# Optimization experiments

Hardware: AMD Instinct MI355X
Metric: run time of the kernel (lower is better)

Reference implementation:

```python
import jax, jax.numpy as jnp
import numpy as np

MARGIN = 0.1
EPS = 1e-6  # torch CosineSimilarity eps


def setup_inputs() -> dict:
    key = jax.random.key(0)
    k1, k2 = jax.random.split(key)
    pred = jax.random.normal(k1, (8192, 512), dtype=jnp.float32)
    labels = jax.random.randint(k2, (8192,), 0, 14)  # one-hot gt <=> int labels
    return {"pred": pred, "labels": labels}


def _cosine(x, y):
    # torch.nn.CosineSimilarity(dim=1, eps=1e-6): clamp norms at eps
    nx = jnp.maximum(jnp.linalg.norm(x, axis=1), EPS)
    ny = jnp.maximum(jnp.linalg.norm(y, axis=1), EPS)
    return jnp.sum(x * y, axis=1) / (nx * ny)


def reference(pred, labels):
    B = pred.shape[0]
    # rows_pos: rows sharing the anchor's label (includes anchor itself, as in torch code)
    pos_mask = labels[:, None] == labels[None, :]  # [B, B] bool
    # random.sample(rows, 1) -> uniform random valid index per row, via gumbel-argmax
    kp, kn = jax.random.split(jax.random.key(42))
    neg_inf = jnp.float32(-1e30)
    g_pos = jax.random.gumbel(kp, (B, B), dtype=jnp.float32)
    g_neg = jax.random.gumbel(kn, (B, B), dtype=jnp.float32)
    idx_p = jnp.argmax(jnp.where(pos_mask, g_pos, neg_inf), axis=1)  # [B]
    idx_n = jnp.argmax(jnp.where(pos_mask, neg_inf, g_neg), axis=1)  # [B]

    anchor = pred
    positive = pred[idx_p]
    negative = pred[idx_n]
    cos_v = _cosine(anchor, positive) - _cosine(anchor, negative) + MARGIN
    return jnp.mean(jnp.maximum(cos_v, 0.0))
```

## Files before the change

### kernel.cpp

```cpp
#include <hip/hip_runtime.h>
#include <stdint.h>


#define B_ROWS 8192
#define DIMS   512
#define NLAB   16

__device__ __forceinline__ uint32_t rotl(uint32_t x, uint32_t r) {
  return __builtin_amdgcn_alignbit(x, x, 32u - r);
}

struct KeyPair { uint32_t a, b; };
constexpr KeyPair tf_c(uint32_t k0, uint32_t k1, uint32_t x0, uint32_t x1) {
  const uint32_t ks2 = k0 ^ k1 ^ 0x1BD11BDAu;
  x0 += k0; x1 += k1;
#define TFRC(r) { x0 += x1; x1 = (uint32_t)((x1 << (r)) | (x1 >> (32 - (r)))); x1 ^= x0; }
  TFRC(13) TFRC(15) TFRC(26) TFRC(6)
  x0 += k1;  x1 += ks2 + 1u;
  TFRC(17) TFRC(29) TFRC(16) TFRC(24)
  x0 += ks2; x1 += k0 + 2u;
  TFRC(13) TFRC(15) TFRC(26) TFRC(6)
  x0 += k0;  x1 += k1 + 3u;
  TFRC(17) TFRC(29) TFRC(16) TFRC(24)
  x0 += k1;  x1 += ks2 + 4u;
  TFRC(13) TFRC(15) TFRC(26) TFRC(6)
  x0 += ks2; x1 += k0 + 5u;
#undef TFRC
  return {x0, x1};
}
constexpr KeyPair KP = tf_c(0u, 42u, 0u, 0u);
constexpr KeyPair KN = tf_c(0u, 42u, 0u, 1u);

template <uint32_t K0, uint32_t K1>
__device__ __forceinline__ uint32_t tf_draw(uint32_t x1) {
  constexpr uint32_t KS2 = K0 ^ K1 ^ 0x1BD11BDAu;
  uint32_t x0 = K0 + x1;
  x1 = rotl(x1, 13); x1 ^= x0;
  x0 += x1; x1 = rotl(x1, 15); x1 ^= x0;
  x0 += x1; x1 = rotl(x1, 26); x1 ^= x0;
  x0 += x1; x1 = rotl(x1, 6);  x1 ^= x0;
  x1 += KS2 + 1u;  x0 = x0 + x1 + K1;
  x1 = rotl(x1, 17); x1 ^= x0;
  x0 += x1; x1 = rotl(x1, 29); x1 ^= x0;
  x0 += x1; x1 = rotl(x1, 16); x1 ^= x0;
  x0 += x1; x1 = rotl(x1, 24); x1 ^= x0;
  x1 += K0 + 2u;   x0 = x0 + x1 + KS2;
  x1 = rotl(x1, 13); x1 ^= x0;
  x0 += x1; x1 = rotl(x1, 15); x1 ^= x0;
  x0 += x1; x1 = rotl(x1, 26); x1 ^= x0;
  x0 += x1; x1 = rotl(x1, 6);  x1 ^= x0;
  x1 += K1 + 3u;   x0 = x0 + x1 + K0;
  x1 = rotl(x1, 17); x1 ^= x0;
  x0 += x1; x1 = rotl(x1, 29); x1 ^= x0;
  x0 += x1; x1 = rotl(x1, 16); x1 ^= x0;
  x0 += x1; x1 = rotl(x1, 24); x1 ^= x0;
  x1 += KS2 + 4u;  x0 = x0 + x1 + K1;
  x1 = rotl(x1, 13); x1 ^= x0;
  x0 += x1; x1 = rotl(x1, 15); x1 ^= x0;
  x0 += x1; x1 = rotl(x1, 26); x1 ^= x0;
  x0 += x1; x1 = rotl(x1, 6);  x1 ^= x0;
  return (x0 + KS2) ^ (x1 + K0 + 5u);
}

__global__ __launch_bounds__(256) void norms_sort_kernel(const float* __restrict__ pred,
                                                         const int* __restrict__ labels,
                                                         float* __restrict__ norms,
                                                         int* __restrict__ perm,
                                                         int* __restrict__ gstart) {
  __shared__ int cnt[NLAB][256];
  __shared__ int gs[NLAB + 1];
  const int wave = threadIdx.x >> 6, lane = threadIdx.x & 63;
  const int r = blockIdx.x * 4 + wave;
  const float4* A = (const float4*)(pred + (size_t)r * DIMS);
  float s = 0.f;
#pragma unroll
  for (int t = 0; t < 2; ++t) {
    const float4 a = A[lane + 64 * t];
    s += a.x * a.x + a.y * a.y + a.z * a.z + a.w * a.w;
  }
  for (int o = 32; o > 0; o >>= 1) s += __shfl_down(s, o, 64);
  if (lane == 0) norms[r] = sqrtf(s);

  if (blockIdx.x != 0) return;
  const int t = threadIdx.x;
  for (int l = 0; l < NLAB; ++l) cnt[l][t] = 0;
  __syncthreads();
  const int base = t * 32;
  for (int e = base; e < base + 32; ++e) cnt[labels[e]][t]++;
  __syncthreads();
  if (t < NLAB) {
    int run = 0;
    for (int k = 0; k < 256; ++k) { const int c = cnt[t][k]; cnt[t][k] = run; run += c; }
    gs[t + 1] = run;
  }
  __syncthreads();
  if (t == 0) {
    gs[0] = 0;
    for (int l = 1; l <= NLAB; ++l) gs[l] += gs[l - 1];
  }
  __syncthreads();
  for (int e = base; e < base + 32; ++e) {
    const int l = labels[e];
    perm[gs[l] + cnt[l][t]++] = e;
  }
  if (t <= NLAB) gstart[t] = gs[t];
}

__global__ __launch_bounds__(256) void argmax_kernel(const int* __restrict__ labels,
                                                     const int* __restrict__ perm,
                                                     const int* __restrict__ gstart,
                                                     int* __restrict__ idxp,
                                                     int* __restrict__ idxn) {
  __shared__ uint32_t labw[B_ROWS / 4];
  const int tid = threadIdx.x;
  {
    const int4* L4 = (const int4*)labels;
#pragma unroll
    for (int q = 0; q < 8; ++q) {
      const int4 a = L4[tid * 8 + q];
      labw[tid * 8 + q] = (uint32_t)a.x | ((uint32_t)a.y << 8) |
                          ((uint32_t)a.z << 16) | ((uint32_t)a.w << 24);
    }
  }
  const int lane = tid & 63;
  const int r = blockIdx.x * 4 + (tid >> 6);
  const int li = __builtin_amdgcn_readfirstlane(labels[r]);
  const int g0 = __builtin_amdgcn_readfirstlane(gstart[li]);
  const int g1 = __builtin_amdgcn_readfirstlane(gstart[li + 1]);
  const uint32_t base = (uint32_t)r << 13;

  int bv = -1, bj = 0;
  {
    const uint32_t sb = base + KP.b;
    for (int t = g0 + lane; t < g1; t += 64) {
      const int j = perm[t];
      const uint32_t w = tf_draw<KP.a, KP.b>(sb + (uint32_t)j);
      const int v = (int)(w >> 9);
      const bool upd = v > bv;
      bv = upd ? v : bv;
      bj = upd ? j : bj;
    }
  }
  unsigned long long pp =
      (((unsigned long long)(bv + 1)) << 13) | (unsigned)(8191 - bj);

  __syncthreads();

  bv = -1; bj = 0;
  {
    const uint8_t* lb = (const uint8_t*)labw;
    uint32_t x1w = base + KN.b + (uint32_t)lane;
    int jw = lane;
#pragma unroll 1
    for (int it = 0; it < 128; it += 8) {
#pragma unroll
      for (int u = 0; u < 8; ++u) {
        const uint32_t w = tf_draw<KN.a, KN.b>(x1w + 64u * u);
        const int lab = (int)lb[jw + 64 * u];
        const int v = (int)(w >> 9);
        const bool upd = (lab != li) & (v > bv);
        bv = upd ? v : bv;
        bj = upd ? (jw + 64 * u) : bj;
      }
      x1w += 512u; jw += 512;
    }
  }
  unsigned long long pn =
      (((unsigned long long)(bv + 1)) << 13) | (unsigned)(8191 - bj);

  for (int o = 32; o > 0; o >>= 1) {
    const unsigned long long t1 = __shfl_down(pp, o, 64); if (t1 > pp) pp = t1;
    const unsigned long long t2 = __shfl_down(pn, o, 64); if (t2 > pn) pn = t2;
  }
  if (lane == 0) {
    idxp[r] = 8191 - (int)(pp & 8191ull);
    idxn[r] = 8191 - (int)(pn & 8191ull);
  }
}

__global__ __launch_bounds__(256) void cos_kernel(const float* __restrict__ pred,
                                                  const float* __restrict__ norms,
                                                  const int* __restrict__ idxp,
                                                  const int* __restrict__ idxn,
                                                  float* __restrict__ cosv) {
  const int wave = threadIdx.x >> 6, lane = threadIdx.x & 63;
  const int r = blockIdx.x * 4 + wave;
  const int ip = idxp[r], inn = idxn[r];
  const float4* A = (const float4*)(pred + (size_t)r * DIMS);
  const float4* P = (const float4*)(pred + (size_t)ip * DIMS);
  const float4* Nn = (const float4*)(pred + (size_t)inn * DIMS);
  float dp = 0.f, dn = 0.f;
#pragma unroll
  for (int t = 0; t < 2; ++t) {
    const float4 a = A[lane + 64 * t];
    const float4 p = P[lane + 64 * t];
    const float4 n = Nn[lane + 64 * t];
    dp += a.x * p.x + a.y * p.y + a.z * p.z + a.w * p.w;
    dn += a.x * n.x + a.y * n.y + a.z * n.z + a.w * n.w;
  }
  for (int o = 32; o > 0; o >>= 1) {
    dp += __shfl_down(dp, o, 64);
    dn += __shfl_down(dn, o, 64);
  }
  if (lane == 0) {
    const float na = fmaxf(norms[r], 1e-6f);
    const float np = fmaxf(norms[ip], 1e-6f);
    const float nn = fmaxf(norms[inn], 1e-6f);
    const float c = dp / (na * np) - dn / (na * nn) + 0.1f;
    cosv[r] = fmaxf(c, 0.f);
  }
}

__global__ __launch_bounds__(256) void reduce_kernel(const float* __restrict__ cosv,
                                                     float* __restrict__ out) {
  __shared__ double sh[4];
  double s = 0.0;
  for (int j = threadIdx.x; j < B_ROWS; j += 256) s += (double)cosv[j];
  for (int o = 32; o > 0; o >>= 1) s += __shfl_down(s, o, 64);
  const int wave = threadIdx.x >> 6, lane = threadIdx.x & 63;
  if (lane == 0) sh[wave] = s;
  __syncthreads();
  if (threadIdx.x == 0) {
    const double t = sh[0] + sh[1] + sh[2] + sh[3];
    out[0] = (float)(t / (double)B_ROWS);
  }
}

extern "C" void kernel_launch(void* const* d_in, const int* in_sizes, int n_in,
                              void* d_out, int out_size, void* d_ws, size_t ws_size,
                              hipStream_t stream) {
  const float* pred  = (const float*)d_in[0];
  const int* labels  = (const int*)d_in[1];
  float* out = (float*)d_out;

  char* ws = (char*)d_ws;
  float* norms  = (float*)(ws + 0);
  int*   idxp   = (int*)(ws + 32 * 1024);
  int*   idxn   = (int*)(ws + 64 * 1024);
  float* cosv   = (float*)(ws + 96 * 1024);
  int*   perm   = (int*)(ws + 128 * 1024);
  int*   gstart = (int*)(ws + 160 * 1024);

  norms_sort_kernel<<<B_ROWS / 4, 256, 0, stream>>>(pred, labels, norms, perm, gstart);
  argmax_kernel<<<B_ROWS / 4, 256, 0, stream>>>(labels, perm, gstart, idxp, idxn);
  cos_kernel<<<B_ROWS / 4, 256, 0, stream>>>(pred, norms, idxp, idxn, cosv);
  reduce_kernel<<<1, 256, 0, stream>>>(cosv, out);
}
```

Measured before the change: 260.1 us.

## Process two rows per wave in argmax, sharing label loads and interleaving Threefry

Each wave now handles two anchor rows in the argmax kernel. The negative-sampling loop computes two Threefry draws side by side, which exposes instruction-level parallelism, and the label reads for each column are shared by both rows. The shared-memory packed-label table and its barrier are removed, and labels are read straight from global memory and served by cache. Half as many blocks are launched, and the higher register use may reduce occupancy.

```diff
diff --git a/kernel.cpp b/kernel.cpp
--- a/kernel.cpp
+++ b/kernel.cpp
@@ -62,6 +62,38 @@
   return (x0 + KS2) ^ (x1 + K0 + 5u);
 }
 
+__device__ __forceinline__ void tf_draw2_kn(uint32_t xa1, uint32_t xb1,
+                                            uint32_t& wa, uint32_t& wb) {
+  constexpr uint32_t K0 = KN.a, K1 = KN.b;
+  constexpr uint32_t KS2 = K0 ^ K1 ^ 0x1BD11BDAu;
+  uint32_t xa0 = K0 + xa1;            uint32_t xb0 = K0 + xb1;
+  xa1 = rotl(xa1, 13);                xb1 = rotl(xb1, 13);
+  xa1 ^= xa0;                         xb1 ^= xb0;
+#define DR(rr) { xa0 += xa1; xb0 += xb1; \
+                 xa1 = rotl(xa1, rr); xb1 = rotl(xb1, rr); \
+                 xa1 ^= xa0; xb1 ^= xb0; }
+  DR(15) DR(26) DR(6)
+  xa1 += KS2 + 1u; xb1 += KS2 + 1u;
+  xa0 = xa0 + xa1 + K1;               xb0 = xb0 + xb1 + K1;
+  xa1 = rotl(xa1, 17); xa1 ^= xa0;    xb1 = rotl(xb1, 17); xb1 ^= xb0;
+  DR(29) DR(16) DR(24)
+  xa1 += K0 + 2u;  xb1 += K0 + 2u;
+  xa0 = xa0 + xa1 + KS2;              xb0 = xb0 + xb1 + KS2;
+  xa1 = rotl(xa1, 13); xa1 ^= xa0;    xb1 = rotl(xb1, 13); xb1 ^= xb0;
+  DR(15) DR(26) DR(6)
+  xa1 += K1 + 3u;  xb1 += K1 + 3u;
+  xa0 = xa0 + xa1 + K0;               xb0 = xb0 + xb1 + K0;
+  xa1 = rotl(xa1, 17); xa1 ^= xa0;    xb1 = rotl(xb1, 17); xb1 ^= xb0;
+  DR(29) DR(16) DR(24)
+  xa1 += KS2 + 4u; xb1 += KS2 + 4u;
+  xa0 = xa0 + xa1 + K1;               xb0 = xb0 + xb1 + K1;
+  xa1 = rotl(xa1, 13); xa1 ^= xa0;    xb1 = rotl(xb1, 13); xb1 ^= xb0;
+  DR(15) DR(26) DR(6)
+#undef DR
+  wa = (xa0 + KS2) ^ (xa1 + K0 + 5u);
+  wb = (xb0 + KS2) ^ (xb1 + K0 + 5u);
+}
+
 __global__ __launch_bounds__(256) void norms_sort_kernel(const float* __restrict__ pred,
                                                          const int* __restrict__ labels,
                                                          float* __restrict__ norms,
@@ -111,70 +143,86 @@
                                                      const int* __restrict__ gstart,
                                                      int* __restrict__ idxp,
                                                      int* __restrict__ idxn) {
-  __shared__ uint32_t labw[B_ROWS / 4];
-  const int tid = threadIdx.x;
+  const int lane = threadIdx.x & 63;
+  const int wave = threadIdx.x >> 6;
+  const int rA = blockIdx.x * 8 + wave;
+  const int rB = rA + 4;
+  const int liA = __builtin_amdgcn_readfirstlane(labels[rA]);
+  const int liB = __builtin_amdgcn_readfirstlane(labels[rB]);
+
+  unsigned long long ppA, ppB;
   {
-    const int4* L4 = (const int4*)labels;
-#pragma unroll
-    for (int q = 0; q < 8; ++q) {
-      const int4 a = L4[tid * 8 + q];
-      labw[tid * 8 + q] = (uint32_t)a.x | ((uint32_t)a.y << 8) |
-                          ((uint32_t)a.z << 16) | ((uint32_t)a.w << 24);
-    }
-  }
-  const int lane = tid & 63;
-  const int r = blockIdx.x * 4 + (tid >> 6);
-  const int li = __builtin_amdgcn_readfirstlane(labels[r]);
-  const int g0 = __builtin_amdgcn_readfirstlane(gstart[li]);
-  const int g1 = __builtin_amdgcn_readfirstlane(gstart[li + 1]);
-  const uint32_t base = (uint32_t)r << 13;
-
-  int bv = -1, bj = 0;
-  {
-    const uint32_t sb = base + KP.b;
+    const int g0 = __builtin_amdgcn_readfirstlane(gstart[liA]);
+    const int g1 = __builtin_amdgcn_readfirstlane(gstart[liA + 1]);
+    const uint32_t sb = ((uint32_t)rA << 13) + KP.b;
+    int bv = -1, bj = 0;
     for (int t = g0 + lane; t < g1; t += 64) {
       const int j = perm[t];
-      const uint32_t w = tf_draw<KP.a, KP.b>(sb + (uint32_t)j);
-      const int v = (int)(w >> 9);
+      const int v = (int)(tf_draw<KP.a, KP.b>(sb + (uint32_t)j) >> 9);
       const bool upd = v > bv;
       bv = upd ? v : bv;
       bj = upd ? j : bj;
     }
-  }
-  unsigned long long pp =
-      (((unsigned long long)(bv + 1)) << 13) | (unsigned)(8191 - bj);
-
-  __syncthreads();
-
-  bv = -1; bj = 0;
+    ppA = (((unsigned long long)(bv + 1)) << 13) | (unsigned)(8191 - bj);
+  }
   {
-    const uint8_t* lb = (const uint8_t*)labw;
-    uint32_t x1w = base + KN.b + (uint32_t)lane;
-    int jw = lane;
+    const int g0 = __builtin_amdgcn_readfirstlane(gstart[liB]);
+    const int g1 = __builtin_amdgcn_readfirstlane(gstart[liB + 1]);
+    const uint32_t sb = ((uint32_t)rB << 13) + KP.b;
+    int bv = -1, bj = 0;
+    for (int t = g0 + lane; t < g1; t += 64) {
+      const int j = perm[t];
+      const int v = (int)(tf_draw<KP.a, KP.b>(sb + (uint32_t)j) >> 9);
+      const bool upd = v > bv;
+      bv = upd ? v : bv;
+      bj = upd ? j : bj;
+    }
+    ppB = (((unsigned long long)(bv + 1)) << 13) | (unsigned)(8191 - bj);
+  }
+
+  int bvA = -1, bjA = 0, bvB = -1, bjB = 0;
+  {
+    const uint32_t sbA = ((uint32_t)rA << 13) + KN.b;
+    const uint32_t sbB = ((uint32_t)rB << 13) + KN.b;
+    int jb = lane;
 #pragma unroll 1
-    for (int it = 0; it < 128; it += 8) {
-#pragma unroll
-      for (int u = 0; u < 8; ++u) {
-        const uint32_t w = tf_draw<KN.a, KN.b>(x1w + 64u * u);
-        const int lab = (int)lb[jw + 64 * u];
-        const int v = (int)(w >> 9);
-        const bool upd = (lab != li) & (v > bv);
-        bv = upd ? v : bv;
-        bj = upd ? (jw + 64 * u) : bj;
+    for (int it = 0; it < 32; ++it) {
+      int lab[4];
+#pragma unroll
+      for (int u = 0; u < 4; ++u) lab[u] = labels[jb + 64 * u];
+#pragma unroll
+      for (int u = 0; u < 4; ++u) {
+        const uint32_t t1 = (uint32_t)(jb + 64 * u);
+        uint32_t wa, wb;
+        tf_draw2_kn(t1 + sbA, t1 + sbB, wa, wb);
+        const int va = (int)(wa >> 9), vb = (int)(wb >> 9);
+        const bool uA = (lab[u] != liA) & (va > bvA);
+        bvA = uA ? va : bvA;
+        bjA = uA ? (jb + 64 * u) : bjA;
+        const bool uB = (lab[u] != liB) & (vb > bvB);
+        bvB = uB ? vb : bvB;
+        bjB = uB ? (jb + 64 * u) : bjB;
       }
-      x1w += 512u; jw += 512;
+      jb += 256;
     }
   }
-  unsigned long long pn =
-      (((unsigned long long)(bv + 1)) << 13) | (unsigned)(8191 - bj);
+  unsigned long long pnA =
+      (((unsigned long long)(bvA + 1)) << 13) | (unsigned)(8191 - bjA);
+  unsigned long long pnB =
+      (((unsigned long long)(bvB + 1)) << 13) | (unsigned)(8191 - bjB);
 
   for (int o = 32; o > 0; o >>= 1) {
-    const unsigned long long t1 = __shfl_down(pp, o, 64); if (t1 > pp) pp = t1;
-    const unsigned long long t2 = __shfl_down(pn, o, 64); if (t2 > pn) pn = t2;
+    unsigned long long t;
+    t = __shfl_down(ppA, o, 64); if (t > ppA) ppA = t;
+    t = __shfl_down(pnA, o, 64); if (t > pnA) pnA = t;
+    t = __shfl_down(ppB, o, 64); if (t > ppB) ppB = t;
+    t = __shfl_down(pnB, o, 64); if (t > pnB) pnB = t;
   }
   if (lane == 0) {
-    idxp[r] = 8191 - (int)(pp & 8191ull);
-    idxn[r] = 8191 - (int)(pn & 8191ull);
+    idxp[rA] = 8191 - (int)(ppA & 8191ull);
+    idxn[rA] = 8191 - (int)(pnA & 8191ull);
+    idxp[rB] = 8191 - (int)(ppB & 8191ull);
+    idxn[rB] = 8191 - (int)(pnB & 8191ull);
   }
 }
 
@@ -242,7 +290,7 @@
   int*   gstart = (int*)(ws + 160 * 1024);
 
   norms_sort_kernel<<<B_ROWS / 4, 256, 0, stream>>>(pred, labels, norms, perm, gstart);
-  argmax_kernel<<<B_ROWS / 4, 256, 0, stream>>>(labels, perm, gstart, idxp, idxn);
+  argmax_kernel<<<B_ROWS / 8, 256, 0, stream>>>(labels, perm, gstart, idxp, idxn);
   cos_kernel<<<B_ROWS / 4, 256, 0, stream>>>(pred, norms, idxp, idxn, cosv);
   reduce_kernel<<<1, 256, 0, stream>>>(cosv, out);
 }
```

Result: no change. 256.7 us (-1.3%).
